# Optimization experiments

Measured on AMD Instinct MI355X. Metric: run time of the kernel, lower is better.

The kernel has to match this reference:

```python
import jax, jax.numpy as jnp
import numpy as np

VOCAB, D = 10000, 32
QUEUE_LEN = 100


def setup_inputs() -> dict:
    key = jax.random.key(0)
    ks = jax.random.split(key, 8)
    B, T = 64, 1024
    s = 0.1
    return dict(
        inputs=jax.random.randint(ks[0], (B, T), 0, 10000, dtype=jnp.int32),
        emb=jax.random.normal(ks[1], (VOCAB, D), dtype=jnp.float32) * s,
        k_lstm=jax.random.normal(ks[2], (D, 4 * D), dtype=jnp.float32) * s,
        rk_lstm=jax.random.normal(ks[3], (D, 4 * D), dtype=jnp.float32) * s,
        b_lstm=jnp.zeros((4 * D,), dtype=jnp.float32),
        W1=jax.random.normal(ks[4], (D, D), dtype=jnp.float32) * s,
        b1=jnp.zeros((D,), dtype=jnp.float32),
        W2=jax.random.normal(ks[5], (D, 1), dtype=jnp.float32) * s,
        b2=jnp.zeros((1,), dtype=jnp.float32),
    )


def _lstm(x, k, rk, b):
    # Keras LSTM, gate order [i, f, g(cell), o], sigmoid recurrent act, tanh act.
    B, T, D = x.shape
    xg = jnp.einsum('btd,de->bte', x, k) + b  # precompute input projections

    def step(carry, xg_t):
        h, c = carry
        z = xg_t + h @ rk
        i, f, g, o = jnp.split(z, 4, axis=-1)
        c = jax.nn.sigmoid(f) * c + jax.nn.sigmoid(i) * jnp.tanh(g)
        h = jax.nn.sigmoid(o) * jnp.tanh(c)
        return (h, c), h

    init = (jnp.zeros((B, D), x.dtype), jnp.zeros((B, D), x.dtype))
    _, hs = jax.lax.scan(step, init, jnp.swapaxes(xg, 0, 1))  # [T,B,D]
    return jnp.swapaxes(hs, 0, 1)  # [B,T,D]


def _zero_index_queue(x_ids):
    # Vectorized replacement of the (i,j) Python scan: last QUEUE_LEN positions
    # (row-major order) where token==0, as [QUEUE_LEN,2] int32, padded with -1.
    B, T = x_ids.shape
    flat = (x_ids == 0).reshape(-1)
    N = flat.shape[0]
    ridx = jnp.nonzero(flat[::-1], size=QUEUE_LEN, fill_value=-1)[0]
    pos = jnp.where(ridx >= 0, N - 1 - ridx, -1)[::-1]  # ascending, like deque
    ii = jnp.where(pos >= 0, pos // T, -1)
    jj = jnp.where(pos >= 0, pos % T, -1)
    return jnp.stack([ii, jj], axis=-1).astype(jnp.int32)


def _forward_float(x_ids, emb, k_lstm, rk_lstm, b_lstm, W1, b1, W2, b2):
    x = emb[x_ids]                                  # [B,T,D]
    h = _lstm(x, k_lstm, rk_lstm, b_lstm)           # [B,T,D]
    scores = jnp.einsum('btd,bsd->bts', h, h)       # unscaled dot attention
    attn = jax.nn.softmax(scores, axis=-1)
    ctx = jnp.einsum('bts,bsd->btd', attn, h)       # Keras Attention output
    y = jnp.einsum('btd,bte->bde', ctx, h)          # Dot(axes=(1,1)) -> [B,D,D]
    y = jax.nn.relu(y @ W1 + b1)
    return jax.nn.sigmoid(y @ W2 + b2)              # [B,D,1]


def reference(inputs, emb, k_lstm, rk_lstm, b_lstm, W1, b1, W2, b2):
    x_ids = jnp.where(inputs < VOCAB, inputs, 0)
    out = _forward_float(x_ids, emb, k_lstm, rk_lstm, b_lstm, W1, b1, W2, b2)
    return out, _zero_index_queue(x_ids)
```

## Files before the change

kernel.cpp:

```cpp
#include <hip/hip_runtime.h>
#include <math.h>

#define BB 64
#define TT 1024
#define DD 32
#define GG 128
#define VOCABN 10000
#define QLEN 100

typedef short short8 __attribute__((ext_vector_type(8)));
typedef float floatx4 __attribute__((ext_vector_type(4)));
typedef float floatx2 __attribute__((ext_vector_type(2)));
typedef unsigned short u16;

__device__ __forceinline__ float fsig(float x) {
    return __builtin_amdgcn_rcpf(1.0f + __expf(-x));
}
__device__ __forceinline__ float readlane_f(float v, int l) {
    return __int_as_float(__builtin_amdgcn_readlane(__float_as_int(v), l));
}
__device__ __forceinline__ u16 f2bf_rne(float x) {
    unsigned u = __float_as_uint(x);
    u += 0x7FFF + ((u >> 16) & 1);
    return (u16)(u >> 16);
}
__device__ __forceinline__ float bf2f(u16 s) {
    return __uint_as_float(((unsigned)s) << 16);
}
__device__ __forceinline__ floatx2 fma2(float s, floatx2 w, floatx2 acc) {
    return __builtin_elementwise_fma((floatx2){s, s}, w, acc);
}

#define UU 8
__global__
__attribute__((amdgpu_flat_work_group_size(128, 128)))
__attribute__((amdgpu_waves_per_eu(1, 1)))
void k_lstm_scan(const int* __restrict__ ids,
                 const float* __restrict__ emb,
                 const float* __restrict__ klstm,
                 const float* __restrict__ bias,
                 const float* __restrict__ rk,
                 float* __restrict__ hout,
                 u16* __restrict__ hh, u16* __restrict__ hl,
                 u16* __restrict__ th, u16* __restrict__ tl,
                 int* __restrict__ list,
                 float* __restrict__ outq) {
    const int b = blockIdx.x;
    const int tid = threadIdx.x;
    const int wv = tid >> 6;
    const int l = tid & 63;
    if (b >= BB) {
        if (wv != 0) return;
        const int4* v4 = (const int4*)ids;
        const int C4 = (BB * TT) / 4 / 64;
        const int b4 = l * C4;
        int cnt = 0;
#pragma unroll 4
        for (int i = 0; i < C4; ++i) {
            int4 v = v4[b4 + i];
            cnt += (v.x == 0 || (unsigned)v.x >= VOCABN);
            cnt += (v.y == 0 || (unsigned)v.y >= VOCABN);
            cnt += (v.z == 0 || (unsigned)v.z >= VOCABN);
            cnt += (v.w == 0 || (unsigned)v.w >= VOCABN);
        }
        int scan = cnt;
#pragma unroll
        for (int o = 1; o < 64; o <<= 1) {
            int nn = __shfl_up(scan, o);
            if (l >= o) scan += nn;
        }
        const int total = __shfl(scan, 63);
        int off = scan - cnt;
        const int base = l * (C4 * 4);
#pragma unroll 4
        for (int i = 0; i < C4; ++i) {
            int4 v = v4[b4 + i];
            if (v.x == 0 || (unsigned)v.x >= VOCABN) list[off++] = base + 4 * i;
            if (v.y == 0 || (unsigned)v.y >= VOCABN) list[off++] = base + 4 * i + 1;
            if (v.z == 0 || (unsigned)v.z >= VOCABN) list[off++] = base + 4 * i + 2;
            if (v.w == 0 || (unsigned)v.w >= VOCABN) list[off++] = base + 4 * i + 3;
        }
        __threadfence();
        const int Kc = total < QLEN ? total : QLEN;
        for (int t = l; t < QLEN; t += 64) {
            float ii = -1.0f, jj = -1.0f;
            if (t >= QLEN - Kc) {
                int pos = list[total - QLEN + t];
                ii = (float)(pos >> 10);
                jj = (float)(pos & (TT - 1));
            }
            outq[2 * t] = ii;
            outq[2 * t + 1] = jj;
        }
        return;
    }

    __shared__ float ring[2][UU][GG];
    __shared__ __align__(16) float hring[2][UU][DD];
    const int* idsb = ids + b * TT;

    if (wv == 1) {
        const int ja = l, jb = l + 64;
        floatx2 kp[DD];
#pragma unroll
        for (int d2 = 0; d2 < DD; ++d2)
            kp[d2] = (floatx2){klstm[d2 * GG + ja], klstm[d2 * GG + jb]};
        const floatx2 bj = (floatx2){bias[ja], bias[jb]};
        const int dd = l & 31;
        const int u_r = l >> 3, dc = (l & 7) * 4;
        const int d_c = l & 31, ug = (l >> 5) * 4;
        u16* hhb = hh + (size_t)b * TT * DD;
        u16* hlb = hl + (size_t)b * TT * DD;
        u16* thb = th + (size_t)b * DD * TT;
        u16* tlb = tl + (size_t)b * DD * TT;

#define PROD_TOKEN(SEL, U, EV)                                               \
        {                                                                    \
            floatx2 z0 = bj;                                                 \
            floatx2 z1 = {0.f, 0.f}, z2 = {0.f, 0.f}, z3 = {0.f, 0.f};       \
            _Pragma("unroll")                                                \
            for (int k = 0; k < DD; k += 4) {                                \
                float e0 = readlane_f(EV, k);                                \
                float e1 = readlane_f(EV, k + 1);                            \
                float e2 = readlane_f(EV, k + 2);                            \
                float e3 = readlane_f(EV, k + 3);                            \
                z0 = fma2(e0, kp[k], z0);                                    \
                z1 = fma2(e1, kp[k + 1], z1);                                \
                z2 = fma2(e2, kp[k + 2], z2);                                \
                z3 = fma2(e3, kp[k + 3], z3);                                \
            }                                                                \
            floatx2 zf = (z0 + z1) + (z2 + z3);                              \
            ring[SEL][U][ja] = zf.x;                                         \
            ring[SEL][U][jb] = zf.y;                                         \
        }

#define CVT_CHUNK(HSEL, TC0)                                                 \
        {                                                                    \
            const float4 hv4 = *(const float4*)&hring[HSEL][u_r][dc];        \
            float xr[4] = {hv4.x, hv4.y, hv4.z, hv4.w};                      \
            u16 rh[4], rl[4];                                                \
            _Pragma("unroll")                                                \
            for (int i = 0; i < 4; ++i) {                                    \
                rh[i] = f2bf_rne(xr[i]);                                     \
                rl[i] = f2bf_rne(xr[i] - bf2f(rh[i]));                       \
            }                                                                \
            ushort4 rhv = {rh[0], rh[1], rh[2], rh[3]};                      \
            ushort4 rlv = {rl[0], rl[1], rl[2], rl[3]};                      \
            *(ushort4*)&hhb[(size_t)((TC0) + u_r) * DD + dc] = rhv;          \
            *(ushort4*)&hlb[(size_t)((TC0) + u_r) * DD + dc] = rlv;          \
            u16 ch[4], cl[4];                                                \
            _Pragma("unroll")                                                \
            for (int j = 0; j < 4; ++j) {                                    \
                float x = hring[HSEL][ug + j][d_c];                          \
                ch[j] = f2bf_rne(x);                                         \
                cl[j] = f2bf_rne(x - bf2f(ch[j]));                           \
            }                                                                \
            ushort4 chv = {ch[0], ch[1], ch[2], ch[3]};                      \
            ushort4 clv = {cl[0], cl[1], cl[2], cl[3]};                      \
            *(ushort4*)&thb[(size_t)d_c * TT + (TC0) + ug] = chv;            \
            *(ushort4*)&tlb[(size_t)d_c * TT + (TC0) + ug] = clv;            \
        }

        {
            int id0 = idsb[0]; if ((unsigned)id0 >= VOCABN) id0 = 0;
            float ec = emb[id0 * DD + dd];
#pragma unroll
            for (int u = 0; u < UU; ++u) {
                float en = 0.f;
                if (u + 1 < UU) {
                    int idn = idsb[u + 1]; if ((unsigned)idn >= VOCABN) idn = 0;
                    en = emb[idn * DD + dd];
                }
                PROD_TOKEN(0, u, ec)
                ec = en;
            }
        }
        __syncthreads();
        int sel = 0;
        for (int t0 = 0; t0 < TT; t0 += UU) {
            if (t0 + UU < TT) {
                const int s = sel ^ 1;
                int id0 = idsb[t0 + UU]; if ((unsigned)id0 >= VOCABN) id0 = 0;
                float ec = emb[id0 * DD + dd];
#pragma unroll
                for (int u = 0; u < UU; ++u) {
                    float en = 0.f;
                    if (u + 1 < UU) {
                        int tn = t0 + UU + u + 1;
                        if (tn > TT - 1) tn = TT - 1;
                        int idn = idsb[tn]; if ((unsigned)idn >= VOCABN) idn = 0;
                        en = emb[idn * DD + dd];
                    }
                    PROD_TOKEN(s, u, ec)
                    ec = en;
                }
            }
            if (t0) CVT_CHUNK((t0 / UU - 1) & 1, t0 - UU)
            __syncthreads();
            sel ^= 1;
        }
        CVT_CHUNK(1, TT - UU)
#undef PROD_TOKEN
#undef CVT_CHUNK
        return;
    }

    const int d = l & 31;
    const bool hi = l >= 32;
    const int ga = (hi ? 32 : 0) + d;
    const int gb = (hi ? 96 : 64) + d;
    floatx2 rkp[DD];
#pragma unroll
    for (int k = 0; k < DD; ++k)
        rkp[k] = (floatx2){rk[k * GG + ga], rk[k * GG + gb]};
    float* hb = hout + (size_t)b * TT * DD;

    float h = 0.0f, c = 0.0f;
    float hreg[UU];
    __syncthreads();
    int sel = 0;
    for (int t0 = 0; t0 < TT; t0 += UU) {
        if (t0 && !hi) {
#pragma unroll
            for (int u = 0; u < UU; ++u) hb[(size_t)(t0 - UU + u) * DD + d] = hreg[u];
        }
        float pa[UU], pb[UU];
#pragma unroll
        for (int u = 0; u < UU; ++u) {
            pa[u] = ring[sel][u][ga];
            pb[u] = ring[sel][u][gb];
        }
#pragma unroll
        for (int u = 0; u < UU; ++u) {
            floatx2 x0 = {pa[u], pb[u]};
            floatx2 x1 = {0.f, 0.f}, x2 = {0.f, 0.f}, x3 = {0.f, 0.f};
#pragma unroll
            for (int k = 0; k < DD; k += 4) {
                float h0 = readlane_f(h, k);
                float h1 = readlane_f(h, k + 1);
                float h2 = readlane_f(h, k + 2);
                float h3 = readlane_f(h, k + 3);
                x0 = fma2(h0, rkp[k],     x0);
                x1 = fma2(h1, rkp[k + 1], x1);
                x2 = fma2(h2, rkp[k + 2], x2);
                x3 = fma2(h3, rkp[k + 3], x3);
            }
            floatx2 zf = (x0 + x1) + (x2 + x3);
            float za = zf.x, zb = zf.y;
            float a = fsig(za);
            float zbm = hi ? zb : 2.0f * zb;
            float s2 = fsig(zbm);
            float bv = hi ? s2 : 2.0f * s2 - 1.0f;
            auto r1 = __builtin_amdgcn_permlane32_swap(
                __float_as_int(bv), __float_as_int(a), false, false);
            auto r2 = __builtin_amdgcn_permlane32_swap(
                __float_as_int(a), __float_as_int(bv), false, false);
            float fg = __int_as_float(r1[0]);
            float og = __int_as_float(r2[0]);
            c = fmaf(fg, c, a * bv);
            float tc = 2.0f * fsig(2.0f * c) - 1.0f;
            h = og * tc;
            hreg[u] = h;
            if (!hi) hring[sel][u][d] = h;
        }
        __syncthreads();
        sel ^= 1;
    }
    if (!hi) {
#pragma unroll
        for (int u = 0; u < UU; ++u) hb[(size_t)(TT - UU + u) * DD + d] = hreg[u];
    }
}

__global__ __launch_bounds__(256, 1) void k_attn(const u16* __restrict__ hh,
                                                 const u16* __restrict__ hl,
                                                 const u16* __restrict__ th,
                                                 const u16* __restrict__ tl,
                                                 float* __restrict__ ctx) {
    __shared__ u16 plds[4][4][2][16 * 40];
    const int tid = threadIdx.x;
    const int w = tid >> 6;
    const int l = tid & 63;
    const int m = l & 15;
    const int g = l >> 4;
    const int b = blockIdx.x & 63;
    const int qt = (blockIdx.x >> 6) * 4 + w;
    const int q0 = qt * 64;
    const size_t rb = (size_t)b * TT * DD;
    const size_t tb = (size_t)b * DD * TT;

    const short8 Qh0 = *(const short8*)&hh[rb + (size_t)(q0 + m) * DD + g * 8];
    const short8 Ql0 = *(const short8*)&hl[rb + (size_t)(q0 + m) * DD + g * 8];
    const short8 Qh1 = *(const short8*)&hh[rb + (size_t)(q0 + 16 + m) * DD + g * 8];
    const short8 Ql1 = *(const short8*)&hl[rb + (size_t)(q0 + 16 + m) * DD + g * 8];
    const short8 Qh2 = *(const short8*)&hh[rb + (size_t)(q0 + 32 + m) * DD + g * 8];
    const short8 Ql2 = *(const short8*)&hl[rb + (size_t)(q0 + 32 + m) * DD + g * 8];
    const short8 Qh3 = *(const short8*)&hh[rb + (size_t)(q0 + 48 + m) * DD + g * 8];
    const short8 Ql3 = *(const short8*)&hl[rb + (size_t)(q0 + 48 + m) * DD + g * 8];
    short8 ONES;
#pragma unroll
    for (int j = 0; j < 8; ++j) ONES[j] = (short)0x3F80;

    floatx4 c0 = {0.f, 0.f, 0.f, 0.f}, c1 = {0.f, 0.f, 0.f, 0.f};
    floatx4 c2 = {0.f, 0.f, 0.f, 0.f}, c3 = {0.f, 0.f, 0.f, 0.f};
    floatx4 c4 = {0.f, 0.f, 0.f, 0.f}, c5 = {0.f, 0.f, 0.f, 0.f};
    floatx4 c6 = {0.f, 0.f, 0.f, 0.f}, c7 = {0.f, 0.f, 0.f, 0.f};
    floatx4 la0 = {0.f, 0.f, 0.f, 0.f}, la1 = {0.f, 0.f, 0.f, 0.f};
    floatx4 la2 = {0.f, 0.f, 0.f, 0.f}, la3 = {0.f, 0.f, 0.f, 0.f};

#define S_BLOCK(QH, QL, KH_A, KL_A, KH_B, KL_B, SA, SB)                       \
    SA = __builtin_amdgcn_mfma_f32_16x16x32_bf16(QH, KH_A, SA, 0, 0, 0);      \
    SA = __builtin_amdgcn_mfma_f32_16x16x32_bf16(QH, KL_A, SA, 0, 0, 0);      \
    SA = __builtin_amdgcn_mfma_f32_16x16x32_bf16(QL, KH_A, SA, 0, 0, 0);      \
    SB = __builtin_amdgcn_mfma_f32_16x16x32_bf16(QH, KH_B, SB, 0, 0, 0);      \
    SB = __builtin_amdgcn_mfma_f32_16x16x32_bf16(QH, KL_B, SB, 0, 0, 0);      \
    SB = __builtin_amdgcn_mfma_f32_16x16x32_bf16(QL, KH_B, SB, 0, 0, 0);

#define EXP_STORE(SA, SB, TILE, SLOT)                                         \
    {                                                                         \
        u16* lp = plds[w][TILE][SLOT];                                        \
        _Pragma("unroll")                                                     \
        for (int r = 0; r < 4; ++r) {                                         \
            lp[(g * 4 + r) * 40 + m]      = f2bf_rne(__expf(SA[r]));          \
            lp[(g * 4 + r) * 40 + 16 + m] = f2bf_rne(__expf(SB[r]));          \
        }                                                                     \
    }

    {
        short8 KhA = *(const short8*)&hh[rb + (size_t)(m) * DD + g * 8];
        short8 KlA = *(const short8*)&hl[rb + (size_t)(m) * DD + g * 8];
        short8 KhB = *(const short8*)&hh[rb + (size_t)(16 + m) * DD + g * 8];
        short8 KlB = *(const short8*)&hl[rb + (size_t)(16 + m) * DD + g * 8];
        floatx4 sA = {0.f, 0.f, 0.f, 0.f}, sB = {0.f, 0.f, 0.f, 0.f};
        floatx4 tA = {0.f, 0.f, 0.f, 0.f}, tB = {0.f, 0.f, 0.f, 0.f};
        floatx4 uA = {0.f, 0.f, 0.f, 0.f}, uB = {0.f, 0.f, 0.f, 0.f};
        floatx4 vA = {0.f, 0.f, 0.f, 0.f}, vB = {0.f, 0.f, 0.f, 0.f};
        S_BLOCK(Qh0, Ql0, KhA, KlA, KhB, KlB, sA, sB)
        S_BLOCK(Qh1, Ql1, KhA, KlA, KhB, KlB, tA, tB)
        S_BLOCK(Qh2, Ql2, KhA, KlA, KhB, KlB, uA, uB)
        S_BLOCK(Qh3, Ql3, KhA, KlA, KhB, KlB, vA, vB)
        EXP_STORE(sA, sB, 0, 0)
        EXP_STORE(tA, tB, 1, 0)
        EXP_STORE(uA, uB, 2, 0)
        EXP_STORE(vA, vB, 3, 0)
    }
    short8 Vh0 = *(const short8*)&th[tb + (size_t)m * TT + g * 8];
    short8 Vl0 = *(const short8*)&tl[tb + (size_t)m * TT + g * 8];
    short8 Vh1 = *(const short8*)&th[tb + (size_t)(16 + m) * TT + g * 8];
    short8 Vl1 = *(const short8*)&tl[tb + (size_t)(16 + m) * TT + g * 8];
    short8 KhA = *(const short8*)&hh[rb + (size_t)(32 + m) * DD + g * 8];
    short8 KlA = *(const short8*)&hl[rb + (size_t)(32 + m) * DD + g * 8];
    short8 KhB = *(const short8*)&hh[rb + (size_t)(48 + m) * DD + g * 8];
    short8 KlB = *(const short8*)&hl[rb + (size_t)(48 + m) * DD + g * 8];

#pragma unroll 1
    for (int kp = 1; kp < 32; ++kp) {
        const int knK = (kp < 31) ? (kp + 1) * 32 : 0;
        const int knV = kp * 32;
        short8 nKhA = *(const short8*)&hh[rb + (size_t)(knK + m) * DD + g * 8];
        short8 nKlA = *(const short8*)&hl[rb + (size_t)(knK + m) * DD + g * 8];
        short8 nKhB = *(const short8*)&hh[rb + (size_t)(knK + 16 + m) * DD + g * 8];
        short8 nKlB = *(const short8*)&hl[rb + (size_t)(knK + 16 + m) * DD + g * 8];
        short8 nVh0 = *(const short8*)&th[tb + (size_t)m * TT + knV + g * 8];
        short8 nVl0 = *(const short8*)&tl[tb + (size_t)m * TT + knV + g * 8];
        short8 nVh1 = *(const short8*)&th[tb + (size_t)(16 + m) * TT + knV + g * 8];
        short8 nVl1 = *(const short8*)&tl[tb + (size_t)(16 + m) * TT + knV + g * 8];

        floatx4 sA = {0.f, 0.f, 0.f, 0.f}, sB = {0.f, 0.f, 0.f, 0.f};
        floatx4 tA = {0.f, 0.f, 0.f, 0.f}, tB = {0.f, 0.f, 0.f, 0.f};
        floatx4 uA = {0.f, 0.f, 0.f, 0.f}, uB = {0.f, 0.f, 0.f, 0.f};
        floatx4 vA = {0.f, 0.f, 0.f, 0.f}, vB = {0.f, 0.f, 0.f, 0.f};
        S_BLOCK(Qh0, Ql0, KhA, KlA, KhB, KlB, sA, sB)
        S_BLOCK(Qh1, Ql1, KhA, KlA, KhB, KlB, tA, tB)
        S_BLOCK(Qh2, Ql2, KhA, KlA, KhB, KlB, uA, uB)
        S_BLOCK(Qh3, Ql3, KhA, KlA, KhB, KlB, vA, vB)

        const int ps = (kp - 1) & 1;
        const short8 P0 = *(const short8*)&plds[w][0][ps][m * 40 + g * 8];
        const short8 P1 = *(const short8*)&plds[w][1][ps][m * 40 + g * 8];
        const short8 P2 = *(const short8*)&plds[w][2][ps][m * 40 + g * 8];
        const short8 P3 = *(const short8*)&plds[w][3][ps][m * 40 + g * 8];

        c0  = __builtin_amdgcn_mfma_f32_16x16x32_bf16(P0, Vh0, c0, 0, 0, 0);
        c0  = __builtin_amdgcn_mfma_f32_16x16x32_bf16(P0, Vl0, c0, 0, 0, 0);
        c1  = __builtin_amdgcn_mfma_f32_16x16x32_bf16(P0, Vh1, c1, 0, 0, 0);
        c1  = __builtin_amdgcn_mfma_f32_16x16x32_bf16(P0, Vl1, c1, 0, 0, 0);
        la0 = __builtin_amdgcn_mfma_f32_16x16x32_bf16(P0, ONES, la0, 0, 0, 0);
        c2  = __builtin_amdgcn_mfma_f32_16x16x32_bf16(P1, Vh0, c2, 0, 0, 0);
        c2  = __builtin_amdgcn_mfma_f32_16x16x32_bf16(P1, Vl0, c2, 0, 0, 0);
        c3  = __builtin_amdgcn_mfma_f32_16x16x32_bf16(P1, Vh1, c3, 0, 0, 0);
        c3  = __builtin_amdgcn_mfma_f32_16x16x32_bf16(P1, Vl1, c3, 0, 0, 0);
        la1 = __builtin_amdgcn_mfma_f32_16x16x32_bf16(P1, ONES, la1, 0, 0, 0);
        c4  = __builtin_amdgcn_mfma_f32_16x16x32_bf16(P2, Vh0, c4, 0, 0, 0);
        c4  = __builtin_amdgcn_mfma_f32_16x16x32_bf16(P2, Vl0, c4, 0, 0, 0);
        c5  = __builtin_amdgcn_mfma_f32_16x16x32_bf16(P2, Vh1, c5, 0, 0, 0);
        c5  = __builtin_amdgcn_mfma_f32_16x16x32_bf16(P2, Vl1, c5, 0, 0, 0);
        la2 = __builtin_amdgcn_mfma_f32_16x16x32_bf16(P2, ONES, la2, 0, 0, 0);
        c6  = __builtin_amdgcn_mfma_f32_16x16x32_bf16(P3, Vh0, c6, 0, 0, 0);
        c6  = __builtin_amdgcn_mfma_f32_16x16x32_bf16(P3, Vl0, c6, 0, 0, 0);
        c7  = __builtin_amdgcn_mfma_f32_16x16x32_bf16(P3, Vh1, c7, 0, 0, 0);
        c7  = __builtin_amdgcn_mfma_f32_16x16x32_bf16(P3, Vl1, c7, 0, 0, 0);
        la3 = __builtin_amdgcn_mfma_f32_16x16x32_bf16(P3, ONES, la3, 0, 0, 0);

        EXP_STORE(sA, sB, 0, kp & 1)
        EXP_STORE(tA, tB, 1, kp & 1)
        EXP_STORE(uA, uB, 2, kp & 1)
        EXP_STORE(vA, vB, 3, kp & 1)

        KhA = nKhA; KlA = nKlA; KhB = nKhB; KlB = nKlB;
        Vh0 = nVh0; Vl0 = nVl0; Vh1 = nVh1; Vl1 = nVl1;
    }
    {
        const short8 P0 = *(const short8*)&plds[w][0][1][m * 40 + g * 8];
        const short8 P1 = *(const short8*)&plds[w][1][1][m * 40 + g * 8];
        const short8 P2 = *(const short8*)&plds[w][2][1][m * 40 + g * 8];
        const short8 P3 = *(const short8*)&plds[w][3][1][m * 40 + g * 8];
        c0  = __builtin_amdgcn_mfma_f32_16x16x32_bf16(P0, Vh0, c0, 0, 0, 0);
        c0  = __builtin_amdgcn_mfma_f32_16x16x32_bf16(P0, Vl0, c0, 0, 0, 0);
        c1  = __builtin_amdgcn_mfma_f32_16x16x32_bf16(P0, Vh1, c1, 0, 0, 0);
        c1  = __builtin_amdgcn_mfma_f32_16x16x32_bf16(P0, Vl1, c1, 0, 0, 0);
        la0 = __builtin_amdgcn_mfma_f32_16x16x32_bf16(P0, ONES, la0, 0, 0, 0);
        c2  = __builtin_amdgcn_mfma_f32_16x16x32_bf16(P1, Vh0, c2, 0, 0, 0);
        c2  = __builtin_amdgcn_mfma_f32_16x16x32_bf16(P1, Vl0, c2, 0, 0, 0);
        c3  = __builtin_amdgcn_mfma_f32_16x16x32_bf16(P1, Vh1, c3, 0, 0, 0);
        c3  = __builtin_amdgcn_mfma_f32_16x16x32_bf16(P1, Vl1, c3, 0, 0, 0);
        la1 = __builtin_amdgcn_mfma_f32_16x16x32_bf16(P1, ONES, la1, 0, 0, 0);
        c4  = __builtin_amdgcn_mfma_f32_16x16x32_bf16(P2, Vh0, c4, 0, 0, 0);
        c4  = __builtin_amdgcn_mfma_f32_16x16x32_bf16(P2, Vl0, c4, 0, 0, 0);
        c5  = __builtin_amdgcn_mfma_f32_16x16x32_bf16(P2, Vh1, c5, 0, 0, 0);
        c5  = __builtin_amdgcn_mfma_f32_16x16x32_bf16(P2, Vl1, c5, 0, 0, 0);
        la2 = __builtin_amdgcn_mfma_f32_16x16x32_bf16(P2, ONES, la2, 0, 0, 0);
        c6  = __builtin_amdgcn_mfma_f32_16x16x32_bf16(P3, Vh0, c6, 0, 0, 0);
        c6  = __builtin_amdgcn_mfma_f32_16x16x32_bf16(P3, Vl0, c6, 0, 0, 0);
        c7  = __builtin_amdgcn_mfma_f32_16x16x32_bf16(P3, Vh1, c7, 0, 0, 0);
        c7  = __builtin_amdgcn_mfma_f32_16x16x32_bf16(P3, Vl1, c7, 0, 0, 0);
        la3 = __builtin_amdgcn_mfma_f32_16x16x32_bf16(P3, ONES, la3, 0, 0, 0);
    }
#undef S_BLOCK
#undef EXP_STORE
#pragma unroll
    for (int r = 0; r < 4; ++r) {
        float li0 = __builtin_amdgcn_rcpf(la0[r]);
        float li1 = __builtin_amdgcn_rcpf(la1[r]);
        float li2 = __builtin_amdgcn_rcpf(la2[r]);
        float li3 = __builtin_amdgcn_rcpf(la3[r]);
        float* cr0 = ctx + (size_t)b * TT * DD + (size_t)(q0 + g * 4 + r) * DD;
        float* cr1 = ctx + (size_t)b * TT * DD + (size_t)(q0 + 16 + g * 4 + r) * DD;
        float* cr2 = ctx + (size_t)b * TT * DD + (size_t)(q0 + 32 + g * 4 + r) * DD;
        float* cr3 = ctx + (size_t)b * TT * DD + (size_t)(q0 + 48 + g * 4 + r) * DD;
        cr0[m]      = c0[r] * li0;
        cr0[16 + m] = c1[r] * li0;
        cr1[m]      = c2[r] * li1;
        cr1[16 + m] = c3[r] * li1;
        cr2[m]      = c4[r] * li2;
        cr2[16 + m] = c5[r] * li2;
        cr3[m]      = c6[r] * li3;
        cr3[16 + m] = c7[r] * li3;
    }
}

__global__ __launch_bounds__(256) void k_ymlp(const float* __restrict__ ctx,
                                              const float* __restrict__ h,
                                              const float* __restrict__ W1,
                                              const float* __restrict__ b1,
                                              const float* __restrict__ W2,
                                              const float* __restrict__ b2,
                                              float* __restrict__ out) {
    const int b = blockIdx.x;
    const int tid = threadIdx.x;
    __shared__ __align__(16) float cs[128 * DD];
    __shared__ __align__(16) float hs[128 * DD];
    const float* cb = ctx + (size_t)b * TT * DD;
    const float* hb = h + (size_t)b * TT * DD;
    const int e = tid & 31;
    const int d4 = (tid >> 5) * 4;
    float acc[4] = {0.f, 0.f, 0.f, 0.f};
    for (int kt = 0; kt < 8; ++kt) {
        const float4* s1 = (const float4*)(cb + (size_t)kt * 128 * DD);
        const float4* s2 = (const float4*)(hb + (size_t)kt * 128 * DD);
        float4* t1 = (float4*)cs;
        float4* t2 = (float4*)hs;
#pragma unroll
        for (int n = 0; n < 4; ++n) {
            t1[tid + n * 256] = s1[tid + n * 256];
            t2[tid + n * 256] = s2[tid + n * 256];
        }
        __syncthreads();
#pragma unroll 2
        for (int s = 0; s < 128; ++s) {
            float hv = hs[s * DD + e];
            float4 cv = *(const float4*)&cs[s * DD + d4];
            acc[0] = fmaf(cv.x, hv, acc[0]);
            acc[1] = fmaf(cv.y, hv, acc[1]);
            acc[2] = fmaf(cv.z, hv, acc[2]);
            acc[3] = fmaf(cv.w, hv, acc[3]);
        }
        __syncthreads();
    }
    __shared__ float ys[DD][DD];
#pragma unroll
    for (int r = 0; r < 4; ++r) ys[d4 + r][e] = acc[r];
    __syncthreads();
    __shared__ float yr[DD][33];
#pragma unroll
    for (int r = 0; r < 4; ++r) {
        float v = b1[e];
#pragma unroll
        for (int ee = 0; ee < DD; ++ee) v += ys[d4 + r][ee] * W1[ee * DD + e];
        yr[d4 + r][e] = fmaxf(v, 0.0f);
    }
    __syncthreads();
    if (tid < DD) {
        float v = b2[0];
#pragma unroll
        for (int ee = 0; ee < DD; ++ee) v += yr[tid][ee] * W2[ee];
        out[b * DD + tid] = 1.0f / (1.0f + expf(-v));
    }
}

extern "C" void kernel_launch(void* const* d_in, const int* in_sizes, int n_in,
                              void* d_out, int out_size, void* d_ws, size_t ws_size,
                              hipStream_t stream) {
    const int* ids   = (const int*)d_in[0];
    const float* emb = (const float*)d_in[1];
    const float* kl  = (const float*)d_in[2];
    const float* rk  = (const float*)d_in[3];
    const float* bl  = (const float*)d_in[4];
    const float* W1  = (const float*)d_in[5];
    const float* b1  = (const float*)d_in[6];
    const float* W2  = (const float*)d_in[7];
    const float* b2  = (const float*)d_in[8];
    float* out = (float*)d_out;

    char* ws = (char*)d_ws;
    const size_t H_ELEMS = (size_t)BB * TT * DD;
    u16* hh   = (u16*)ws;
    u16* hl   = (u16*)(ws + H_ELEMS * 2);
    u16* th   = (u16*)(ws + H_ELEMS * 4);
    u16* tl   = (u16*)(ws + H_ELEMS * 6);
    float* h  = (float*)(ws + H_ELEMS * 8);
    float* ctx = (float*)(ws + H_ELEMS * 8 + H_ELEMS * 4);
    int* list = (int*)(ws + H_ELEMS * 8 + H_ELEMS * 8);

    k_lstm_scan<<<BB + 1, 128, 0, stream>>>(ids, emb, kl, bl, rk, h,
                                            hh, hl, th, tl, list, out + BB * DD);
    k_attn<<<BB * 4, 256, 0, stream>>>(hh, hl, th, tl, ctx);
    k_ymlp<<<BB, 256, 0, stream>>>(ctx, h, W1, b1, W2, b2, out);
}
```

Measured before the change: 383.1 us.

## Compute ctx^T·h contraction with split-bf16 MFMA using transposed ctx layout

The attention kernel now writes ctx transposed ([D,T] per batch) as a hi/lo bf16 pair instead of fp32 rows. The y = ctx^T h reduction kernel then runs on MFMA 16x16x32 bf16 instructions with three-term split precision, reading the transposed hi/lo h buffers. Each of the four waves covers a quarter of T, and the partial results are summed in shared memory. This replaces a scalar FMA loop with LDS staging, at the cost of scattered 2-byte transposed stores from k_attn and a small loss of precision from the dropped lo*lo term.

```diff
diff --git a/kernel.cpp b/kernel.cpp
--- a/kernel.cpp
+++ b/kernel.cpp
@@ -276,7 +276,8 @@
                                                  const u16* __restrict__ hl,
                                                  const u16* __restrict__ th,
                                                  const u16* __restrict__ tl,
-                                                 float* __restrict__ ctx) {
+                                                 u16* __restrict__ cth,
+                                                 u16* __restrict__ ctl) {
     __shared__ u16 plds[4][4][2][16 * 40];
     const int tid = threadIdx.x;
     const int w = tid >> 6;
@@ -438,29 +439,39 @@
     }
 #undef S_BLOCK
 #undef EXP_STORE
+#define CTX_STORE(VAL, DROW, TCOL)                                            \
+    {                                                                         \
+        float v_ = (VAL);                                                     \
+        u16 h_ = f2bf_rne(v_);                                                \
+        cth[tb + (size_t)(DROW) * TT + (TCOL)] = h_;                          \
+        ctl[tb + (size_t)(DROW) * TT + (TCOL)] = f2bf_rne(v_ - bf2f(h_));     \
+    }
 #pragma unroll
     for (int r = 0; r < 4; ++r) {
         float li0 = __builtin_amdgcn_rcpf(la0[r]);
         float li1 = __builtin_amdgcn_rcpf(la1[r]);
         float li2 = __builtin_amdgcn_rcpf(la2[r]);
         float li3 = __builtin_amdgcn_rcpf(la3[r]);
-        float* cr0 = ctx + (size_t)b * TT * DD + (size_t)(q0 + g * 4 + r) * DD;
-        float* cr1 = ctx + (size_t)b * TT * DD + (size_t)(q0 + 16 + g * 4 + r) * DD;
-        float* cr2 = ctx + (size_t)b * TT * DD + (size_t)(q0 + 32 + g * 4 + r) * DD;
-        float* cr3 = ctx + (size_t)b * TT * DD + (size_t)(q0 + 48 + g * 4 + r) * DD;
-        cr0[m]      = c0[r] * li0;
-        cr0[16 + m] = c1[r] * li0;
-        cr1[m]      = c2[r] * li1;
-        cr1[16 + m] = c3[r] * li1;
-        cr2[m]      = c4[r] * li2;
-        cr2[16 + m] = c5[r] * li2;
-        cr3[m]      = c6[r] * li3;
-        cr3[16 + m] = c7[r] * li3;
-    }
-}
-
-__global__ __launch_bounds__(256) void k_ymlp(const float* __restrict__ ctx,
-                                              const float* __restrict__ h,
+        const int ta = q0 + g * 4 + r;
+        const int tbr = q0 + 16 + g * 4 + r;
+        const int tc = q0 + 32 + g * 4 + r;
+        const int td = q0 + 48 + g * 4 + r;
+        CTX_STORE(c0[r] * li0, m, ta)
+        CTX_STORE(c1[r] * li0, 16 + m, ta)
+        CTX_STORE(c2[r] * li1, m, tbr)
+        CTX_STORE(c3[r] * li1, 16 + m, tbr)
+        CTX_STORE(c4[r] * li2, m, tc)
+        CTX_STORE(c5[r] * li2, 16 + m, tc)
+        CTX_STORE(c6[r] * li3, m, td)
+        CTX_STORE(c7[r] * li3, 16 + m, td)
+    }
+#undef CTX_STORE
+}
+
+__global__ __launch_bounds__(256) void k_ymlp(const u16* __restrict__ cth,
+                                              const u16* __restrict__ ctl,
+                                              const u16* __restrict__ th,
+                                              const u16* __restrict__ tl,
                                               const float* __restrict__ W1,
                                               const float* __restrict__ b1,
                                               const float* __restrict__ W2,
@@ -468,38 +479,55 @@
                                               float* __restrict__ out) {
     const int b = blockIdx.x;
     const int tid = threadIdx.x;
-    __shared__ __align__(16) float cs[128 * DD];
-    __shared__ __align__(16) float hs[128 * DD];
-    const float* cb = ctx + (size_t)b * TT * DD;
-    const float* hb = h + (size_t)b * TT * DD;
+    const int w = tid >> 6;
+    const int l = tid & 63;
+    const int m = l & 15;
+    const int g = l >> 4;
+    const size_t tb = (size_t)b * DD * TT;
+    const int k0 = w * (TT / 4);
+
+    floatx4 y00 = {0.f, 0.f, 0.f, 0.f}, y01 = {0.f, 0.f, 0.f, 0.f};
+    floatx4 y10 = {0.f, 0.f, 0.f, 0.f}, y11 = {0.f, 0.f, 0.f, 0.f};
+#pragma unroll 2
+    for (int ks = 0; ks < TT / 4; ks += 32) {
+        const size_t kk = (size_t)(k0 + ks + g * 8);
+        short8 A0h = *(const short8*)&cth[tb + (size_t)m * TT + kk];
+        short8 A0l = *(const short8*)&ctl[tb + (size_t)m * TT + kk];
+        short8 A1h = *(const short8*)&cth[tb + (size_t)(16 + m) * TT + kk];
+        short8 A1l = *(const short8*)&ctl[tb + (size_t)(16 + m) * TT + kk];
+        short8 B0h = *(const short8*)&th[tb + (size_t)m * TT + kk];
+        short8 B0l = *(const short8*)&tl[tb + (size_t)m * TT + kk];
+        short8 B1h = *(const short8*)&th[tb + (size_t)(16 + m) * TT + kk];
+        short8 B1l = *(const short8*)&tl[tb + (size_t)(16 + m) * TT + kk];
+        y00 = __builtin_amdgcn_mfma_f32_16x16x32_bf16(A0h, B0h, y00, 0, 0, 0);
+        y00 = __builtin_amdgcn_mfma_f32_16x16x32_bf16(A0h, B0l, y00, 0, 0, 0);
+        y00 = __builtin_amdgcn_mfma_f32_16x16x32_bf16(A0l, B0h, y00, 0, 0, 0);
+        y01 = __builtin_amdgcn_mfma_f32_16x16x32_bf16(A0h, B1h, y01, 0, 0, 0);
+        y01 = __builtin_amdgcn_mfma_f32_16x16x32_bf16(A0h, B1l, y01, 0, 0, 0);
+        y01 = __builtin_amdgcn_mfma_f32_16x16x32_bf16(A0l, B1h, y01, 0, 0, 0);
+        y10 = __builtin_amdgcn_mfma_f32_16x16x32_bf16(A1h, B0h, y10, 0, 0, 0);
+        y10 = __builtin_amdgcn_mfma_f32_16x16x32_bf16(A1h, B0l, y10, 0, 0, 0);
+        y10 = __builtin_amdgcn_mfma_f32_16x16x32_bf16(A1l, B0h, y10, 0, 0, 0);
+        y11 = __builtin_amdgcn_mfma_f32_16x16x32_bf16(A1h, B1h, y11, 0, 0, 0);
+        y11 = __builtin_amdgcn_mfma_f32_16x16x32_bf16(A1h, B1l, y11, 0, 0, 0);
+        y11 = __builtin_amdgcn_mfma_f32_16x16x32_bf16(A1l, B1h, y11, 0, 0, 0);
+    }
+    __shared__ float ysp[4][DD][DD];
+#pragma unroll
+    for (int r = 0; r < 4; ++r) {
+        ysp[w][g * 4 + r][m]           = y00[r];
+        ysp[w][g * 4 + r][16 + m]      = y01[r];
+        ysp[w][16 + g * 4 + r][m]      = y10[r];
+        ysp[w][16 + g * 4 + r][16 + m] = y11[r];
+    }
+    __syncthreads();
     const int e = tid & 31;
     const int d4 = (tid >> 5) * 4;
-    float acc[4] = {0.f, 0.f, 0.f, 0.f};
-    for (int kt = 0; kt < 8; ++kt) {
-        const float4* s1 = (const float4*)(cb + (size_t)kt * 128 * DD);
-        const float4* s2 = (const float4*)(hb + (size_t)kt * 128 * DD);
-        float4* t1 = (float4*)cs;
-        float4* t2 = (float4*)hs;
-#pragma unroll
-        for (int n = 0; n < 4; ++n) {
-            t1[tid + n * 256] = s1[tid + n * 256];
-            t2[tid + n * 256] = s2[tid + n * 256];
-        }
-        __syncthreads();
-#pragma unroll 2
-        for (int s = 0; s < 128; ++s) {
-            float hv = hs[s * DD + e];
-            float4 cv = *(const float4*)&cs[s * DD + d4];
-            acc[0] = fmaf(cv.x, hv, acc[0]);
-            acc[1] = fmaf(cv.y, hv, acc[1]);
-            acc[2] = fmaf(cv.z, hv, acc[2]);
-            acc[3] = fmaf(cv.w, hv, acc[3]);
-        }
-        __syncthreads();
-    }
     __shared__ float ys[DD][DD];
 #pragma unroll
-    for (int r = 0; r < 4; ++r) ys[d4 + r][e] = acc[r];
+    for (int r = 0; r < 4; ++r)
+        ys[d4 + r][e] = (ysp[0][d4 + r][e] + ysp[1][d4 + r][e])
+                      + (ysp[2][d4 + r][e] + ysp[3][d4 + r][e]);
     __syncthreads();
     __shared__ float yr[DD][33];
 #pragma unroll
@@ -539,11 +567,12 @@
     u16* th   = (u16*)(ws + H_ELEMS * 4);
     u16* tl   = (u16*)(ws + H_ELEMS * 6);
     float* h  = (float*)(ws + H_ELEMS * 8);
-    float* ctx = (float*)(ws + H_ELEMS * 8 + H_ELEMS * 4);
+    u16* cth  = (u16*)(ws + H_ELEMS * 8 + H_ELEMS * 4);
+    u16* ctl  = (u16*)(ws + H_ELEMS * 8 + H_ELEMS * 4 + H_ELEMS * 2);
     int* list = (int*)(ws + H_ELEMS * 8 + H_ELEMS * 8);
 
     k_lstm_scan<<<BB + 1, 128, 0, stream>>>(ids, emb, kl, bl, rk, h,
                                             hh, hl, th, tl, list, out + BB * DD);
-    k_attn<<<BB * 4, 256, 0, stream>>>(hh, hl, th, tl, ctx);
-    k_ymlp<<<BB, 256, 0, stream>>>(ctx, h, W1, b1, W2, b2, out);
-}
+    k_attn<<<BB * 4, 256, 0, stream>>>(hh, hl, th, tl, cth, ctl);
+    k_ymlp<<<BB, 256, 0, stream>>>(cth, ctl, th, tl, W1, b1, W2, b2, out);
+}
```

Result: faster. 366.5 us (-4.3%).
